# Performance work log

Measured on AMD Instinct MI355X. Metric: run time of the kernel, lower is better.

Reference implementation:

```python
import jax, jax.numpy as jnp
import numpy as np

NUM_NODES = 100_000
NUM_EDGES = 1_200_000
NUM_REL = 3
EMBED_DIM = 64
HIDDEN_DIM = 64
NUM_CLS = 2
NUM_GRAPHS = 512


def setup_inputs() -> dict:
    key = jax.random.key(0)
    ks = jax.random.split(key, 12)
    s = 1.0 / np.sqrt(EMBED_DIM)
    inp = {
        # forward args
        "x": jnp.zeros((NUM_NODES,), dtype=jnp.int64),  # vocab size 1 -> all zeros
        "edge_index": jax.random.randint(ks[0], (2, NUM_EDGES), 0, NUM_NODES, dtype=jnp.int64),
        "edge_type": jax.random.randint(ks[1], (NUM_EDGES,), 0, NUM_REL, dtype=jnp.int64),
        "batch": jnp.sort(jax.random.randint(ks[2], (NUM_NODES,), 0, NUM_GRAPHS, dtype=jnp.int64)),
        # parameters
        "embed_w": jax.random.normal(ks[3], (1, EMBED_DIM), jnp.float32),
        "W1": jax.random.normal(ks[4], (NUM_REL, EMBED_DIM, HIDDEN_DIM), jnp.float32) * s,
        "root1": jax.random.normal(ks[5], (EMBED_DIM, HIDDEN_DIM), jnp.float32) * s,
        "b1": jnp.zeros((HIDDEN_DIM,), jnp.float32),
        "W2": jax.random.normal(ks[6], (NUM_REL, HIDDEN_DIM, HIDDEN_DIM), jnp.float32) * s,
        "root2": jax.random.normal(ks[7], (HIDDEN_DIM, HIDDEN_DIM), jnp.float32) * s,
        "b2": jnp.zeros((HIDDEN_DIM,), jnp.float32),
        "lin_w": jax.random.normal(ks[8], (HIDDEN_DIM, NUM_CLS), jnp.float32) * s,
        "lin_b": jnp.zeros((NUM_CLS,), jnp.float32),
    }
    return inp


def rgcn_conv(h, W, root, b, src, dst, edge_type):
    """PyG RGCNConv with mean aggregation per relation + root weight + bias."""
    n = h.shape[0]
    out = h @ root + b  # root/self contribution, [N, H]
    for r in range(NUM_REL):
        m = (edge_type == r).astype(h.dtype)  # [E]
        tr = h @ W[r]                          # [N, H] small GEMM
        msg = tr[src] * m[:, None]             # gather [E, H]
        ssum = jax.ops.segment_sum(msg, dst, num_segments=n)  # scatter-add [N, H]
        cnt = jax.ops.segment_sum(m, dst, num_segments=n)     # per-relation in-degree
        out = out + ssum / jnp.clip(cnt, 1.0)[:, None]        # mean aggregation
    return out


def reference(x, edge_index, edge_type, batch, embed_w, W1, root1, b1, W2, root2, b2, lin_w, lin_b):
    src, dst = edge_index[0], edge_index[1]
    h = embed_w[x]                                       # [N, D] embedding lookup
    h = jax.nn.relu(rgcn_conv(h, W1, root1, b1, src, dst, edge_type))
    h = jax.nn.relu(rgcn_conv(h, W2, root2, b2, src, dst, edge_type))
    # global mean pool over graphs
    gsum = jax.ops.segment_sum(h, batch, num_segments=NUM_GRAPHS)            # [G, H]
    gcnt = jax.ops.segment_sum(jnp.ones_like(h[:, 0]), batch, num_segments=NUM_GRAPHS)
    g_emb = gsum / jnp.clip(gcnt, 1.0)[:, None]
    return g_emb @ lin_w + lin_b                          # [G, num_cls]
```

## Files before the change

kernel.cpp:

```cpp
#include <hip/hip_runtime.h>

#define NODES   100000
#define EDGES   1200000
#define NREL    3
#define DIM     64
#define NGRAPH  512

#define BSH     8
#define NB      391
#define BUCKCAP 4096
#define SBLK    256
#define CHUNK   4688
#define MBPITCH 100352

#define OFF_GSUM  0
#define OFF_GCNT  131072
#define OFF_CUR   133120
#define OFF_MB    135168
#define OFF_ZEND  436224
#define OFF_CNT   436224
#define OFF_MASK  2836224
#define OFF_REC   2936576
#define OFF_H1    9342720
#define OFF_BASE  9344768
#define OFF_T2    9346816

__global__ void k_tab1(const float* __restrict__ embed_w, const float* __restrict__ W1,
                       const float* __restrict__ root1, const float* __restrict__ b1,
                       float* __restrict__ H1) {
    __shared__ float h0[DIM];
    __shared__ float u[DIM];
    __shared__ float t[NREL][DIM];
    const int tid = threadIdx.x;
    const int j = tid & 63, w = tid >> 6;
    if (tid < DIM) h0[tid] = embed_w[tid];
    __syncthreads();
    const float* M = (w == 0) ? root1 : (W1 + (size_t)(w - 1) * DIM * DIM);
    float s = 0.f;
    for (int k = 0; k < DIM; ++k) s += h0[k] * M[k * DIM + j];
    if (w == 0) u[j] = s + b1[j];
    else        t[w - 1][j] = s;
    __syncthreads();
    for (int p = w; p < 8; p += 4) {
        float v = u[j];
        if (p & 1) v += t[0][j];
        if (p & 2) v += t[1][j];
        if (p & 4) v += t[2][j];
        H1[p * DIM + j] = fmaxf(v, 0.f);
    }
}

__global__ void k_tab2(const float* __restrict__ H1, const float* __restrict__ root2,
                       const float* __restrict__ b2, const float* __restrict__ W2,
                       float* __restrict__ base, float* __restrict__ T2,
                       char* __restrict__ ws) {
    {
        uint4* z = (uint4*)ws;
        const uint4 zz = make_uint4(0, 0, 0, 0);
        const int gt = blockIdx.x * 256 + threadIdx.x;
        for (int i = gt; i < OFF_ZEND / 16; i += 8192) z[i] = zz;
    }
    __shared__ float hrow[DIM];
    __shared__ float red[4][DIM];
    const int tid = threadIdx.x;
    const int j = tid & 63, kq = tid >> 6;
    const int row = blockIdx.x;
    const int p = (row < 8) ? row : ((row - 8) & 7);
    if (tid < DIM) hrow[tid] = H1[p * DIM + tid];
    __syncthreads();
    const float* M = (row < 8) ? root2 : (W2 + (size_t)((row - 8) >> 3) * DIM * DIM);
    float s = 0.f;
    for (int k = kq * 16; k < kq * 16 + 16; ++k) s += hrow[k] * M[k * DIM + j];
    red[kq][j] = s;
    __syncthreads();
    if (kq == 0) {
        const float v = red[0][j] + red[1][j] + red[2][j] + red[3][j];
        if (row < 8) base[p * DIM + j] = v + b2[j];
        else         T2[(row - 8) * DIM + j] = v;
    }
}

__global__ void k_scatter(const int* __restrict__ ei, const int* __restrict__ et,
                          int* __restrict__ cursor, unsigned int* __restrict__ rec,
                          unsigned char* __restrict__ mb) {
    __shared__ int hist[NB];
    __shared__ int cur[NB];
    const int tid = threadIdx.x;
    for (int b = tid; b < NB; b += 256) hist[b] = 0;
    __syncthreads();
    const int e0 = blockIdx.x * CHUNK;
    const int* src = ei;
    const int* dst = ei + EDGES;
    for (int i = tid; i < CHUNK / 4; i += 256) {
        const int e = e0 + i * 4;
        if (e < EDGES) {
            const int4 d4 = *(const int4*)(dst + e);
            atomicAdd(&hist[d4.x >> BSH], 1);
            atomicAdd(&hist[d4.y >> BSH], 1);
            atomicAdd(&hist[d4.z >> BSH], 1);
            atomicAdd(&hist[d4.w >> BSH], 1);
        }
    }
    __syncthreads();
    for (int b = tid; b < NB; b += 256) {
        const int h = hist[b];
        const int r = h ? atomicAdd(&cursor[b], h) : 0;
        cur[b] = b * BUCKCAP + r;
    }
    __syncthreads();
    for (int i = tid; i < CHUNK / 4; i += 256) {
        const int e = e0 + i * 4;
        if (e < EDGES) {
            const int4 s4 = *(const int4*)(src + e);
            const int4 d4 = *(const int4*)(dst + e);
            const int4 r4 = *(const int4*)(et + e);
            int p;
            p = atomicAdd(&cur[d4.x >> BSH], 1);
            if (p < ((d4.x >> BSH) + 1) * BUCKCAP)
                rec[p] = ((unsigned)(d4.x & 255) << 19) | ((unsigned)r4.x << 17) | (unsigned)s4.x;
            mb[r4.x * MBPITCH + d4.x] = 1;
            p = atomicAdd(&cur[d4.y >> BSH], 1);
            if (p < ((d4.y >> BSH) + 1) * BUCKCAP)
                rec[p] = ((unsigned)(d4.y & 255) << 19) | ((unsigned)r4.y << 17) | (unsigned)s4.y;
            mb[r4.y * MBPITCH + d4.y] = 1;
            p = atomicAdd(&cur[d4.z >> BSH], 1);
            if (p < ((d4.z >> BSH) + 1) * BUCKCAP)
                rec[p] = ((unsigned)(d4.z & 255) << 19) | ((unsigned)r4.z << 17) | (unsigned)s4.z;
            mb[r4.z * MBPITCH + d4.z] = 1;
            p = atomicAdd(&cur[d4.w >> BSH], 1);
            if (p < ((d4.w >> BSH) + 1) * BUCKCAP)
                rec[p] = ((unsigned)(d4.w & 255) << 19) | ((unsigned)r4.w << 17) | (unsigned)s4.w;
            mb[r4.w * MBPITCH + d4.w] = 1;
        }
    }
}

__global__ void k_asm(const unsigned char* __restrict__ mb,
                      unsigned char* __restrict__ mask) {
    const int v = (blockIdx.x * blockDim.x + threadIdx.x) * 4;
    if (v >= NODES) return;
    const uchar4 a = *(const uchar4*)(mb + v);
    const uchar4 b = *(const uchar4*)(mb + MBPITCH + v);
    const uchar4 c = *(const uchar4*)(mb + 2 * MBPITCH + v);
    uchar4 o;
    o.x = (unsigned char)(a.x | (b.x << 1) | (c.x << 2));
    o.y = (unsigned char)(a.y | (b.y << 1) | (c.y << 2));
    o.z = (unsigned char)(a.z | (b.z << 1) | (c.z << 2));
    o.w = (unsigned char)(a.w | (b.w << 1) | (c.w << 2));
    *(uchar4*)(mask + v) = o;
}

__global__ void k_hist(const unsigned int* __restrict__ rec, const int* __restrict__ cursor,
                       const unsigned char* __restrict__ mask,
                       unsigned long long* __restrict__ cnt) {
    __shared__ unsigned int h[256 * 24 / 2];
    const int tid = threadIdx.x;
    for (int i = tid; i < 3072; i += 256) h[i] = 0;
    __syncthreads();
    const int b = blockIdx.x;
    const int s = b * BUCKCAP;
    int n = cursor[b];
    if (n > BUCKCAP) n = BUCKCAP;
    for (int i = tid; i < n; i += 256) {
        const unsigned r32 = rec[s + i];
        const int idx = (r32 >> 19) * 24 + ((r32 >> 17) & 3) * 8 + mask[r32 & 0x1FFFF];
        atomicAdd(&h[idx >> 1], 1u << ((idx & 1) * 16));
    }
    __syncthreads();
    const int v = (b << BSH) + tid;
    if (v < NODES) {
        const int w0 = tid * 12;
        for (int r = 0; r < NREL; ++r) {
            unsigned long long w = 0;
            #pragma unroll
            for (int q = 0; q < 4; ++q) {
                const unsigned x = h[w0 + r * 4 + q];
                w |= ((unsigned long long)(x & 0xFFFFu) << (16 * q))
                   | ((unsigned long long)(x >> 16)    << (16 * q + 8));
            }
            cnt[(size_t)v * 3 + r] = w;
        }
    }
}

__global__ void k_node(const unsigned char* __restrict__ mask,
                       const unsigned long long* __restrict__ cnt,
                       const int* __restrict__ batch,
                       const float* __restrict__ base, const float* __restrict__ T2,
                       float* __restrict__ gsum, int* __restrict__ gcnt) {
    __shared__ float bs[8 * DIM];
    __shared__ float ts[24 * DIM];
    const int tid = threadIdx.x;
    for (int i = tid; i < 8 * DIM; i += 256) bs[i] = base[i];
    for (int i = tid; i < 24 * DIM; i += 256) ts[i] = T2[i];
    __syncthreads();
    const int lane = tid & 63;
    const int grp = blockIdx.x * 4 + (tid >> 6);
    const int v0 = grp * 8;
    if (v0 >= NODES) return;
    float acc = 0.f;
    int curg = -1, runlen = 0;
    for (int i = 0; i < 8; ++i) {
        const int v = v0 + i;
        if (v >= NODES) break;
        float s = bs[mask[v] * DIM + lane];
        for (int r = 0; r < NREL; ++r) {
            const unsigned long long w = cnt[(size_t)v * 3 + r];
            float msg = 0.f;
            int cr = 0;
            #pragma unroll
            for (int p = 0; p < 8; ++p) {
                const int c = (int)((w >> (8 * p)) & 0xFF);
                cr += c;
                msg += (float)c * ts[(r * 8 + p) * DIM + lane];
            }
            s += msg / fmaxf((float)cr, 1.0f);
        }
        s = fmaxf(s, 0.f);
        const int g = batch[v];
        if (g != curg) {
            if (curg >= 0) {
                atomicAdd(&gsum[curg * DIM + lane], acc);
                if (lane == 0) atomicAdd(&gcnt[curg], runlen);
            }
            curg = g; acc = 0.f; runlen = 0;
        }
        acc += s; runlen++;
    }
    if (curg >= 0) {
        atomicAdd(&gsum[curg * DIM + lane], acc);
        if (lane == 0) atomicAdd(&gcnt[curg], runlen);
    }
}

__global__ void k_final(const float* __restrict__ gsum, const int* __restrict__ gcnt,
                        const float* __restrict__ lin_w, const float* __restrict__ lin_b,
                        float* __restrict__ out) {
    const int lane = threadIdx.x & 63;
    const int g = blockIdx.x * (blockDim.x >> 6) + (threadIdx.x >> 6);
    if (g >= NGRAPH) return;
    const float inv = 1.0f / fmaxf((float)gcnt[g], 1.0f);
    const float s = gsum[g * DIM + lane] * inv;
    float p0 = s * lin_w[lane * 2 + 0];
    float p1 = s * lin_w[lane * 2 + 1];
    for (int off = 32; off; off >>= 1) {
        p0 += __shfl_down(p0, off);
        p1 += __shfl_down(p1, off);
    }
    if (lane == 0) {
        out[g * 2 + 0] = p0 + lin_b[0];
        out[g * 2 + 1] = p1 + lin_b[1];
    }
}

extern "C" void kernel_launch(void* const* d_in, const int* in_sizes, int n_in,
                              void* d_out, int out_size, void* d_ws, size_t ws_size,
                              hipStream_t stream) {
    const int*   ei      = (const int*)d_in[1];
    const int*   et      = (const int*)d_in[2];
    const int*   batch   = (const int*)d_in[3];
    const float* embed_w = (const float*)d_in[4];
    const float* W1      = (const float*)d_in[5];
    const float* root1   = (const float*)d_in[6];
    const float* b1      = (const float*)d_in[7];
    const float* W2      = (const float*)d_in[8];
    const float* root2   = (const float*)d_in[9];
    const float* b2      = (const float*)d_in[10];
    const float* lin_w   = (const float*)d_in[11];
    const float* lin_b   = (const float*)d_in[12];
    float* out = (float*)d_out;

    char* ws = (char*)d_ws;
    float*              gsum = (float*)(ws + OFF_GSUM);
    int*                gcnt = (int*)(ws + OFF_GCNT);
    int*                cur  = (int*)(ws + OFF_CUR);
    unsigned char*      mb   = (unsigned char*)(ws + OFF_MB);
    unsigned long long* cnt  = (unsigned long long*)(ws + OFF_CNT);
    unsigned char*      mask = (unsigned char*)(ws + OFF_MASK);
    unsigned int*       rec  = (unsigned int*)(ws + OFF_REC);
    float*              H1   = (float*)(ws + OFF_H1);
    float*              base = (float*)(ws + OFF_BASE);
    float*              T2   = (float*)(ws + OFF_T2);

    k_tab1   <<<1,    256, 0, stream>>>(embed_w, W1, root1, b1, H1);
    k_tab2   <<<32,   256, 0, stream>>>(H1, root2, b2, W2, base, T2, ws);
    k_scatter<<<SBLK, 256, 0, stream>>>(ei, et, cur, rec, mb);
    k_asm    <<<98,   256, 0, stream>>>(mb, mask);
    k_hist   <<<NB,   256, 0, stream>>>(rec, cur, mask, cnt);
    k_node   <<<3125, 256, 0, stream>>>(mask, cnt, batch, base, T2, gsum, gcnt);
    k_final  <<<128,  256, 0, stream>>>(gsum, gcnt, lin_w, lin_b, out);
}
```

Measured before the change: 157.4 us.

## Fuse table kernels and merge histogram with node aggregation in shared memory

The two weight-table kernels become one, with every block recomputing the layer-1 table redundantly. The mask-assembly, histogram and node kernels are fused into one 512-thread-per-bucket kernel. That kernel reads the per-relation byte flags directly and consumes the shared-memory counts in place, so the global count array and mask no longer need to be written and read back. This cuts launches and global round trips, but the node stage now runs on only 391 blocks with 32 nodes per wavefront, which lowers parallelism there.

```diff
diff --git a/kernel.cpp b/kernel.cpp
--- a/kernel.cpp
+++ b/kernel.cpp
@@ -18,71 +18,64 @@
 #define OFF_CUR   133120
 #define OFF_MB    135168
 #define OFF_ZEND  436224
-#define OFF_CNT   436224
-#define OFF_MASK  2836224
-#define OFF_REC   2936576
-#define OFF_H1    9342720
-#define OFF_BASE  9344768
-#define OFF_T2    9346816
-
-__global__ void k_tab1(const float* __restrict__ embed_w, const float* __restrict__ W1,
-                       const float* __restrict__ root1, const float* __restrict__ b1,
-                       float* __restrict__ H1) {
+#define OFF_REC   436224
+#define OFF_BASE  6842368
+#define OFF_T2    6844416
+
+__global__ void k_tab(const float* __restrict__ embed_w, const float* __restrict__ W1,
+                      const float* __restrict__ root1, const float* __restrict__ b1,
+                      const float* __restrict__ W2, const float* __restrict__ root2,
+                      const float* __restrict__ b2,
+                      float* __restrict__ base, float* __restrict__ T2,
+                      char* __restrict__ ws) {
+    {
+        uint4* z = (uint4*)ws;
+        const uint4 zz = make_uint4(0, 0, 0, 0);
+        const int gt = blockIdx.x * 256 + threadIdx.x;
+        for (int i = gt; i < OFF_ZEND / 16; i += 32 * 256) z[i] = zz;
+    }
     __shared__ float h0[DIM];
     __shared__ float u[DIM];
     __shared__ float t[NREL][DIM];
+    __shared__ float h1s[8][DIM];
+    __shared__ float red[4][DIM];
     const int tid = threadIdx.x;
     const int j = tid & 63, w = tid >> 6;
     if (tid < DIM) h0[tid] = embed_w[tid];
     __syncthreads();
-    const float* M = (w == 0) ? root1 : (W1 + (size_t)(w - 1) * DIM * DIM);
-    float s = 0.f;
-    for (int k = 0; k < DIM; ++k) s += h0[k] * M[k * DIM + j];
-    if (w == 0) u[j] = s + b1[j];
-    else        t[w - 1][j] = s;
+    {
+        const float* M = (w == 0) ? root1 : (W1 + (size_t)(w - 1) * DIM * DIM);
+        float s = 0.f;
+        for (int k = 0; k < DIM; ++k) s += h0[k] * M[k * DIM + j];
+        if (w == 0) u[j] = s + b1[j];
+        else        t[w - 1][j] = s;
+    }
     __syncthreads();
     for (int p = w; p < 8; p += 4) {
         float v = u[j];
         if (p & 1) v += t[0][j];
         if (p & 2) v += t[1][j];
         if (p & 4) v += t[2][j];
-        H1[p * DIM + j] = fmaxf(v, 0.f);
-    }
-}
-
-__global__ void k_tab2(const float* __restrict__ H1, const float* __restrict__ root2,
-                       const float* __restrict__ b2, const float* __restrict__ W2,
-                       float* __restrict__ base, float* __restrict__ T2,
-                       char* __restrict__ ws) {
-    {
-        uint4* z = (uint4*)ws;
-        const uint4 zz = make_uint4(0, 0, 0, 0);
-        const int gt = blockIdx.x * 256 + threadIdx.x;
-        for (int i = gt; i < OFF_ZEND / 16; i += 8192) z[i] = zz;
-    }
-    __shared__ float hrow[DIM];
-    __shared__ float red[4][DIM];
-    const int tid = threadIdx.x;
-    const int j = tid & 63, kq = tid >> 6;
+        h1s[p][j] = fmaxf(v, 0.f);
+    }
+    __syncthreads();
     const int row = blockIdx.x;
     const int p = (row < 8) ? row : ((row - 8) & 7);
-    if (tid < DIM) hrow[tid] = H1[p * DIM + tid];
-    __syncthreads();
     const float* M = (row < 8) ? root2 : (W2 + (size_t)((row - 8) >> 3) * DIM * DIM);
     float s = 0.f;
-    for (int k = kq * 16; k < kq * 16 + 16; ++k) s += hrow[k] * M[k * DIM + j];
-    red[kq][j] = s;
-    __syncthreads();
-    if (kq == 0) {
+    for (int k = w * 16; k < w * 16 + 16; ++k) s += h1s[p][k] * M[k * DIM + j];
+    red[w][j] = s;
+    __syncthreads();
+    if (w == 0) {
         const float v = red[0][j] + red[1][j] + red[2][j] + red[3][j];
         if (row < 8) base[p * DIM + j] = v + b2[j];
         else         T2[(row - 8) * DIM + j] = v;
     }
 }
 
-__global__ void k_scatter(const int* __restrict__ ei, const int* __restrict__ et,
-                          int* __restrict__ cursor, unsigned int* __restrict__ rec,
-                          unsigned char* __restrict__ mb) {
+__global__ void k_scat(const int* __restrict__ ei, const int* __restrict__ et,
+                       int* __restrict__ cursor, unsigned int* __restrict__ rec,
+                       unsigned char* __restrict__ mb) {
     __shared__ int hist[NB];
     __shared__ int cur[NB];
     const int tid = threadIdx.x;
@@ -135,88 +128,57 @@
     }
 }
 
-__global__ void k_asm(const unsigned char* __restrict__ mb,
-                      unsigned char* __restrict__ mask) {
-    const int v = (blockIdx.x * blockDim.x + threadIdx.x) * 4;
-    if (v >= NODES) return;
-    const uchar4 a = *(const uchar4*)(mb + v);
-    const uchar4 b = *(const uchar4*)(mb + MBPITCH + v);
-    const uchar4 c = *(const uchar4*)(mb + 2 * MBPITCH + v);
-    uchar4 o;
-    o.x = (unsigned char)(a.x | (b.x << 1) | (c.x << 2));
-    o.y = (unsigned char)(a.y | (b.y << 1) | (c.y << 2));
-    o.z = (unsigned char)(a.z | (b.z << 1) | (c.z << 2));
-    o.w = (unsigned char)(a.w | (b.w << 1) | (c.w << 2));
-    *(uchar4*)(mask + v) = o;
-}
-
-__global__ void k_hist(const unsigned int* __restrict__ rec, const int* __restrict__ cursor,
-                       const unsigned char* __restrict__ mask,
-                       unsigned long long* __restrict__ cnt) {
-    __shared__ unsigned int h[256 * 24 / 2];
+__global__ void k_histnode(const unsigned int* __restrict__ rec,
+                           const int* __restrict__ cursor,
+                           const unsigned char* __restrict__ mb,
+                           const int* __restrict__ batch,
+                           const float* __restrict__ base, const float* __restrict__ T2,
+                           float* __restrict__ gsum, int* __restrict__ gcnt) {
+    __shared__ unsigned int h[3072];
+    __shared__ float bs[8 * DIM];
+    __shared__ float ts[24 * DIM];
     const int tid = threadIdx.x;
-    for (int i = tid; i < 3072; i += 256) h[i] = 0;
+    for (int i = tid; i < 3072; i += 512) h[i] = 0;
+    for (int i = tid; i < 8 * DIM; i += 512) bs[i] = base[i];
+    for (int i = tid; i < 24 * DIM; i += 512) ts[i] = T2[i];
     __syncthreads();
     const int b = blockIdx.x;
     const int s = b * BUCKCAP;
     int n = cursor[b];
     if (n > BUCKCAP) n = BUCKCAP;
-    for (int i = tid; i < n; i += 256) {
+    for (int i = tid; i < n; i += 512) {
         const unsigned r32 = rec[s + i];
-        const int idx = (r32 >> 19) * 24 + ((r32 >> 17) & 3) * 8 + mask[r32 & 0x1FFFF];
+        const int sv = r32 & 0x1FFFF;
+        const int p = mb[sv] | (mb[MBPITCH + sv] << 1) | (mb[2 * MBPITCH + sv] << 2);
+        const int idx = (r32 >> 19) * 24 + ((r32 >> 17) & 3) * 8 + p;
         atomicAdd(&h[idx >> 1], 1u << ((idx & 1) * 16));
     }
     __syncthreads();
-    const int v = (b << BSH) + tid;
-    if (v < NODES) {
-        const int w0 = tid * 12;
-        for (int r = 0; r < NREL; ++r) {
-            unsigned long long w = 0;
-            #pragma unroll
-            for (int q = 0; q < 4; ++q) {
-                const unsigned x = h[w0 + r * 4 + q];
-                w |= ((unsigned long long)(x & 0xFFFFu) << (16 * q))
-                   | ((unsigned long long)(x >> 16)    << (16 * q + 8));
-            }
-            cnt[(size_t)v * 3 + r] = w;
-        }
-    }
-}
-
-__global__ void k_node(const unsigned char* __restrict__ mask,
-                       const unsigned long long* __restrict__ cnt,
-                       const int* __restrict__ batch,
-                       const float* __restrict__ base, const float* __restrict__ T2,
-                       float* __restrict__ gsum, int* __restrict__ gcnt) {
-    __shared__ float bs[8 * DIM];
-    __shared__ float ts[24 * DIM];
-    const int tid = threadIdx.x;
-    for (int i = tid; i < 8 * DIM; i += 256) bs[i] = base[i];
-    for (int i = tid; i < 24 * DIM; i += 256) ts[i] = T2[i];
-    __syncthreads();
     const int lane = tid & 63;
-    const int grp = blockIdx.x * 4 + (tid >> 6);
-    const int v0 = grp * 8;
-    if (v0 >= NODES) return;
+    const int w = tid >> 6;
+    const int v0 = (b << BSH) + w * 32;
     float acc = 0.f;
     int curg = -1, runlen = 0;
-    for (int i = 0; i < 8; ++i) {
+    for (int i = 0; i < 32; ++i) {
         const int v = v0 + i;
         if (v >= NODES) break;
-        float s = bs[mask[v] * DIM + lane];
+        const int pm = mb[v] | (mb[MBPITCH + v] << 1) | (mb[2 * MBPITCH + v] << 2);
+        float sacc = bs[pm * DIM + lane];
+        const unsigned* hv = &h[(v & 255) * 12];
         for (int r = 0; r < NREL; ++r) {
-            const unsigned long long w = cnt[(size_t)v * 3 + r];
             float msg = 0.f;
             int cr = 0;
             #pragma unroll
-            for (int p = 0; p < 8; ++p) {
-                const int c = (int)((w >> (8 * p)) & 0xFF);
-                cr += c;
-                msg += (float)c * ts[(r * 8 + p) * DIM + lane];
+            for (int q = 0; q < 4; ++q) {
+                const unsigned x = hv[r * 4 + q];
+                const int c0 = (int)(x & 0xFFFFu), c1 = (int)(x >> 16);
+                cr += c0 + c1;
+                msg += (float)c0 * ts[(r * 8 + 2 * q) * DIM + lane]
+                     + (float)c1 * ts[(r * 8 + 2 * q + 1) * DIM + lane];
             }
-            s += msg / fmaxf((float)cr, 1.0f);
-        }
-        s = fmaxf(s, 0.f);
+            sacc += msg / fmaxf((float)cr, 1.0f);
+        }
+        sacc = fmaxf(sacc, 0.f);
         const int g = batch[v];
         if (g != curg) {
             if (curg >= 0) {
@@ -225,7 +187,7 @@
             }
             curg = g; acc = 0.f; runlen = 0;
         }
-        acc += s; runlen++;
+        acc += sacc; runlen++;
     }
     if (curg >= 0) {
         atomicAdd(&gsum[curg * DIM + lane], acc);
@@ -271,22 +233,17 @@
     float* out = (float*)d_out;
 
     char* ws = (char*)d_ws;
-    float*              gsum = (float*)(ws + OFF_GSUM);
-    int*                gcnt = (int*)(ws + OFF_GCNT);
-    int*                cur  = (int*)(ws + OFF_CUR);
-    unsigned char*      mb   = (unsigned char*)(ws + OFF_MB);
-    unsigned long long* cnt  = (unsigned long long*)(ws + OFF_CNT);
-    unsigned char*      mask = (unsigned char*)(ws + OFF_MASK);
-    unsigned int*       rec  = (unsigned int*)(ws + OFF_REC);
-    float*              H1   = (float*)(ws + OFF_H1);
-    float*              base = (float*)(ws + OFF_BASE);
-    float*              T2   = (float*)(ws + OFF_T2);
-
-    k_tab1   <<<1,    256, 0, stream>>>(embed_w, W1, root1, b1, H1);
-    k_tab2   <<<32,   256, 0, stream>>>(H1, root2, b2, W2, base, T2, ws);
-    k_scatter<<<SBLK, 256, 0, stream>>>(ei, et, cur, rec, mb);
-    k_asm    <<<98,   256, 0, stream>>>(mb, mask);
-    k_hist   <<<NB,   256, 0, stream>>>(rec, cur, mask, cnt);
-    k_node   <<<3125, 256, 0, stream>>>(mask, cnt, batch, base, T2, gsum, gcnt);
-    k_final  <<<128,  256, 0, stream>>>(gsum, gcnt, lin_w, lin_b, out);
-}
+    float*         gsum = (float*)(ws + OFF_GSUM);
+    int*           gcnt = (int*)(ws + OFF_GCNT);
+    int*           cur  = (int*)(ws + OFF_CUR);
+    unsigned char* mb   = (unsigned char*)(ws + OFF_MB);
+    unsigned int*  rec  = (unsigned int*)(ws + OFF_REC);
+    float*         base = (float*)(ws + OFF_BASE);
+    float*         T2   = (float*)(ws + OFF_T2);
+
+    k_tab     <<<32,   256, 0, stream>>>(embed_w, W1, root1, b1, W2, root2, b2,
+                                         base, T2, ws);
+    k_scat    <<<SBLK, 256, 0, stream>>>(ei, et, cur, rec, mb);
+    k_histnode<<<NB,   512, 0, stream>>>(rec, cur, mb, batch, base, T2, gsum, gcnt);
+    k_final   <<<128,  256, 0, stream>>>(gsum, gcnt, lin_w, lin_b, out);
+}
```

Measured after the change: 163.3 us. 3.7% more time.
